# Kernel optimization log

Hardware: AMD Instinct MI355X
Metric: run time of the kernel (lower is better)

The kernel has to match this reference:

```python
import jax, jax.numpy as jnp
import numpy as np

IN_DIM, OUT_DIM = 96, 32
D = IN_DIM + OUT_DIM  # 128, feature dim of x
H, KQ = 8, 64         # head_num, KQ_dim
GAMMA = 1e-4


def setup_inputs() -> dict:
    key = jax.random.key(0)
    kx, kk, kq, kv = jax.random.split(key, 4)
    B, N = 32, 2048
    std_kq = (GAMMA / D) ** 0.5
    return {
        "x": jax.random.normal(kx, (B, N, D), dtype=jnp.float32),
        # nn.Linear weight shape [out_features, in_features]; stacked per head
        "Wk": jax.random.normal(kk, (H, KQ, D), dtype=jnp.float32) * std_kq,
        "Wq": jax.random.normal(kq, (H, KQ, D), dtype=jnp.float32) * std_kq,
        "Wv": jax.random.normal(kv, (H, D, D), dtype=jnp.float32) * GAMMA,
    }


def reference(x, Wk, Wq, Wv):
    # Per-head projections (nn.Linear: y = x @ W^T), stacked over heads h
    K = jnp.einsum("bnd,hkd->bhnk", x, Wk)  # [B,H,N,KQ]
    Q = jnp.einsum("bnd,hkd->bhnk", x, Wq)  # [B,H,N,KQ]
    V = jnp.einsum("bnd,hed->bhne", x, Wv)  # [B,H,N,D]
    # No softmax -> (Q K^T) V == Q (K^T V); use the O(n d^2) associative form
    KtV = jnp.einsum("bhnk,bhne->bhke", K, V)  # [B,H,KQ,D]
    # sum over heads folded into the contraction
    out = jnp.einsum("bhnk,bhke->bne", Q, KtV)  # [B,N,D]
    return out
```

## Files before the change

### kernel.cpp

```cpp
#include <hip/hip_runtime.h>

#define BB 32
#define NN 2048
#define DD 128
#define HH 8
#define KK 64

typedef __attribute__((ext_vector_type(8))) short bf16x8;
typedef __attribute__((ext_vector_type(4))) float f32x4;
#define MFMA_BF16 __builtin_amdgcn_mfma_f32_16x16x32_bf16


__device__ __forceinline__ float bf2f(unsigned short h){ return __uint_as_float(((unsigned)h) << 16); }
__device__ __forceinline__ unsigned short f2bf(float f){
  unsigned u = __float_as_uint(f);
  u += 0x7fffu + ((u >> 16) & 1u);
  return (unsigned short)(u >> 16);
}
__device__ __forceinline__ unsigned pack2(float a, float b){
  return (unsigned)f2bf(a) | ((unsigned)f2bf(b) << 16);
}

__device__ __forceinline__ bf16x8 ldfrag_sw(const unsigned short* base, int row16, int kc, int lane){
  int d = row16 + (lane & 15);
  int q = lane >> 4;
  int ch = ((kc << 2) + q) ^ (d & 7);
  return *(const bf16x8*)(base + d*128 + ch*8);
}

__global__ __launch_bounds__(512, 4) void kgkp(const float* __restrict__ x,
                                               const float* __restrict__ Wq,
                                               const float* __restrict__ Wk,
                                               unsigned short* __restrict__ Gp_bf,
                                               unsigned short* __restrict__ Pbf){
  __shared__ __align__(16) unsigned short sm[32768];
  const int t = threadIdx.x;
  const int bid = blockIdx.x;
  const int w = t >> 6, lane = t & 63, quad = lane >> 4;
  if (bid < 256){
    unsigned short* xh = sm;
    unsigned short* xl = sm + 16384;
    const int b = bid & 31, chunk = bid >> 5;
    const int wr = (w >> 1)*32, wc = (w & 1)*64;
    f32x4 acc[2][4] = {};
    for (int sub = 0; sub < 2; ++sub){
      if (sub) __syncthreads();
      const float* xb = x + ((size_t)b*NN + (size_t)(chunk*256 + sub*128))*DD;
      for (int it = 0; it < 2; ++it){
        int gidx = it*512 + t;
        int n4g = (gidx & 7) | (((gidx >> 6) & 3) << 3);
        int dcq = ((gidx >> 3) & 7) | (((gidx >> 8) & 3) << 3);
        float4 v[4];
        #pragma unroll
        for (int j = 0; j < 4; ++j)
          v[j] = *(const float4*)(xb + (size_t)(n4g*4 + j)*DD + dcq*4);
        #pragma unroll
        for (int i = 0; i < 4; ++i){
          int d = dcq*4 + i;
          float f0 = (&v[0].x)[i], f1 = (&v[1].x)[i], f2 = (&v[2].x)[i], f3 = (&v[3].x)[i];
          unsigned short h0 = f2bf(f0), h1 = f2bf(f1), h2 = f2bf(f2), h3 = f2bf(f3);
          unsigned short l0 = f2bf(f0 - bf2f(h0)), l1 = f2bf(f1 - bf2f(h1));
          unsigned short l2 = f2bf(f2 - bf2f(h2)), l3 = f2bf(f3 - bf2f(h3));
          int off = d*128 + ((((n4g >> 1) ^ (d & 7)) << 3) + (n4g & 1)*4);
          *(ushort4*)(xh + off) = make_ushort4(h0, h1, h2, h3);
          *(ushort4*)(xl + off) = make_ushort4(l0, l1, l2, l3);
        }
      }
      __syncthreads();
      for (int kc = 0; kc < 4; ++kc){
        bf16x8 ah[2], al[2], bh[4], bl[4];
        #pragma unroll
        for (int r = 0; r < 2; ++r){
          ah[r] = ldfrag_sw(xh, wr + r*16, kc, lane);
          al[r] = ldfrag_sw(xl, wr + r*16, kc, lane);
        }
        #pragma unroll
        for (int c = 0; c < 4; ++c){
          bh[c] = ldfrag_sw(xh, wc + c*16, kc, lane);
          bl[c] = ldfrag_sw(xl, wc + c*16, kc, lane);
        }
        #pragma unroll
        for (int r = 0; r < 2; ++r)
          #pragma unroll
          for (int c = 0; c < 4; ++c){
            acc[r][c] = MFMA_BF16(ah[r], bh[c], acc[r][c], 0, 0, 0);
            acc[r][c] = MFMA_BF16(ah[r], bl[c], acc[r][c], 0, 0, 0);
            acc[r][c] = MFMA_BF16(al[r], bh[c], acc[r][c], 0, 0, 0);
          }
      }
    }
    __syncthreads();
    float* Sf = (float*)sm;
    #pragma unroll
    for (int r = 0; r < 2; ++r)
      #pragma unroll
      for (int c = 0; c < 4; ++c)
        #pragma unroll
        for (int reg = 0; reg < 4; ++reg)
          Sf[(wr + r*16 + quad*4 + reg)*128 + wc + c*16 + (lane & 15)] = acc[r][c][reg];
    __syncthreads();
    unsigned short* gp = Gp_bf + ((size_t)(chunk*32 + b) << 14);
    for (int i = t; i < 2048; i += 512){
      int r = i >> 4, c8 = (i & 15) * 8;
      const float* s = Sf + r*128 + c8;
      uint4 o;
      o.x = pack2(s[0], s[1]); o.y = pack2(s[2], s[3]);
      o.z = pack2(s[4], s[5]); o.w = pack2(s[6], s[7]);
      *(uint4*)(gp + r*128 + c8) = o;
    }
  } else {
    float* Aq = (float*)sm;
    float* Bk = Aq + 64*36;
    const int kpid = bid - 256;
    const int h = kpid >> 2, rt = kpid & 3;
    const int i0 = rt * 32;
    const int tr = t >> 6, tc = t & 63;
    const float* wq = Wq + h*KK*DD;
    const float* wk = Wk + h*KK*DD;
    for (int i = t; i < 512; i += 512){
      int k = i >> 3, c4 = (i & 7) << 2;
      *(float4*)(&Aq[k*36 + c4]) = *(const float4*)(wq + k*DD + i0 + c4);
    }
    for (int i = t; i < 2048; i += 512){
      int k = i >> 5, c4 = (i & 31) << 2;
      *(float4*)(&Bk[k*132 + c4]) = *(const float4*)(wk + k*DD + c4);
    }
    __syncthreads();
    float acc[4][2] = {};
    for (int k = 0; k < 64; k += 2){
      float a0[4], a1[4], b0[2], b1[2];
      *(float4*)a0 = *(float4*)(&Aq[k*36 + tr*4]);
      *(float4*)a1 = *(float4*)(&Aq[(k+1)*36 + tr*4]);
      b0[0] = Bk[k*132 + tc*2];     b0[1] = Bk[k*132 + tc*2 + 1];
      b1[0] = Bk[(k+1)*132 + tc*2]; b1[1] = Bk[(k+1)*132 + tc*2 + 1];
      #pragma unroll
      for (int i = 0; i < 4; ++i)
        #pragma unroll
        for (int j = 0; j < 2; ++j){
          acc[i][j] += a0[i]*b0[j];
          acc[i][j] += a1[i]*b1[j];
        }
    }
    unsigned short* Ph = Pbf + h*DD*DD;
    #pragma unroll
    for (int i = 0; i < 4; ++i)
      *(ushort2*)(&Ph[(i0 + tr*4 + i)*DD + tc*2]) =
          make_ushort2(f2bf(acc[i][0]), f2bf(acc[i][1]));
  }
}

__global__ __launch_bounds__(512, 2) void km2(const unsigned short* __restrict__ Gp_bf,
                                              const float* __restrict__ Wv,
                                              const unsigned short* __restrict__ Pbf,
                                              unsigned short* __restrict__ Mp_bf){
  __shared__ __align__(16) unsigned short sm[32768];
  unsigned short* As = sm;
  unsigned short* Bs = sm + 16384;
  const int bid = blockIdx.x;
  const int b = bid & 31, h = bid >> 5;
  const int t = threadIdx.x;
  const int w = t >> 6, lane = t & 63, quad = lane >> 4;
  for (int i = t; i < 2048; i += 512){
    int r = i >> 4, c8 = (i & 15) * 8;
    float s[8] = {};
    #pragma unroll
    for (int p = 0; p < 8; ++p){
      uint4 u = *(const uint4*)(Gp_bf + (((size_t)(p*32 + b)) << 14) + r*128 + c8);
      const unsigned short* pu = (const unsigned short*)&u;
      #pragma unroll
      for (int j = 0; j < 8; ++j) s[j] += bf2f(pu[j]);
    }
    uint4 o;
    o.x = pack2(s[0], s[1]); o.y = pack2(s[2], s[3]);
    o.z = pack2(s[4], s[5]); o.w = pack2(s[6], s[7]);
    *(uint4*)(As + r*128 + ((((c8 >> 3) ^ (r & 7))) << 3)) = o;
  }
  const float* Wvh = Wv + (size_t)h*DD*DD;
  for (int i = t; i < 4096; i += 512){
    int e = i >> 5, dc = (i & 31) * 4;
    float4 v = *(const float4*)(Wvh + (size_t)e*DD + dc);
    int off = e*128 + ((((dc >> 3) ^ (e & 7)) << 3) + (dc & 4));
    *(ushort4*)(Bs + off) = make_ushort4(f2bf(v.x), f2bf(v.y), f2bf(v.z), f2bf(v.w));
  }
  __syncthreads();
  f32x4 acc1[8] = {};
  for (int kc = 0; kc < 4; ++kc){
    bf16x8 a = ldfrag_sw(As, w*16, kc, lane);
    bf16x8 bb[8];
    #pragma unroll
    for (int c = 0; c < 8; ++c) bb[c] = ldfrag_sw(Bs, c*16, kc, lane);
    #pragma unroll
    for (int c = 0; c < 8; ++c) acc1[c] = MFMA_BF16(a, bb[c], acc1[c], 0, 0, 0);
  }
  __syncthreads();
  #pragma unroll
  for (int c = 0; c < 8; ++c){
    int e = c*16 + (lane & 15);
    int d0 = w*16 + quad*4;
    int off = e*128 + ((((d0 >> 3) ^ (e & 7)) << 3) + (d0 & 7));
    *(ushort4*)(Bs + off) = make_ushort4(f2bf(acc1[c][0]), f2bf(acc1[c][1]),
                                         f2bf(acc1[c][2]), f2bf(acc1[c][3]));
  }
  const unsigned short* Ph = Pbf + (size_t)h*DD*DD;
  for (int i = t; i < 2048; i += 512){
    int r = i >> 4, ch = i & 15;
    *(uint4*)(As + r*128 + ((ch ^ (r & 7)) << 3)) = *(const uint4*)(Ph + r*128 + ch*8);
  }
  __syncthreads();
  f32x4 acc2[8] = {};
  for (int kc = 0; kc < 4; ++kc){
    bf16x8 a = ldfrag_sw(As, w*16, kc, lane);
    bf16x8 bb[8];
    #pragma unroll
    for (int c = 0; c < 8; ++c) bb[c] = ldfrag_sw(Bs, c*16, kc, lane);
    #pragma unroll
    for (int c = 0; c < 8; ++c) acc2[c] = MFMA_BF16(a, bb[c], acc2[c], 0, 0, 0);
  }
  __syncthreads();
  float* Sf = (float*)sm;
  #pragma unroll
  for (int c = 0; c < 8; ++c)
    #pragma unroll
    for (int reg = 0; reg < 4; ++reg)
      Sf[(w*16 + quad*4 + reg)*128 + c*16 + (lane & 15)] = acc2[c][reg];
  __syncthreads();
  unsigned short* Mb = Mp_bf + (((size_t)(b*8 + h)) << 14);
  for (int i = t; i < 2048; i += 512){
    int r = i >> 4, c8 = (i & 15) * 8;
    const float* s = Sf + r*128 + c8;
    uint4 o;
    o.x = pack2(s[0], s[1]); o.y = pack2(s[2], s[3]);
    o.z = pack2(s[4], s[5]); o.w = pack2(s[6], s[7]);
    *(uint4*)(Mb + r*128 + c8) = o;
  }
}

__global__ __launch_bounds__(256) void kmr(const unsigned short* __restrict__ Mp_bf,
                                           unsigned short* __restrict__ Mtbf){
  __shared__ float Sf[16][132];
  const int bid = blockIdx.x;
  const int b = bid >> 3, es = bid & 7;
  const int t = threadIdx.x;
  {
    int d = t >> 1, half = t & 1;
    float s[8] = {};
    #pragma unroll
    for (int h = 0; h < 8; ++h){
      uint4 u = *(const uint4*)(Mp_bf + (((size_t)(b*8 + h)) << 14) + d*128 + es*16 + half*8);
      const unsigned short* pu = (const unsigned short*)&u;
      #pragma unroll
      for (int j = 0; j < 8; ++j) s[j] += bf2f(pu[j]);
    }
    #pragma unroll
    for (int j = 0; j < 8; ++j) Sf[half*8 + j][d] = s[j];
  }
  __syncthreads();
  unsigned short* Mb = Mtbf + ((size_t)b << 14);
  for (int j = t; j < 2048; j += 256){
    int e = j >> 7, d = j & 127;
    Mb[(es*16 + e)*128 + d] = f2bf(Sf[e][d]);
  }
}

__global__ __launch_bounds__(512, 4) void ko2(const float* __restrict__ x,
                                              const unsigned short* __restrict__ Mtbf,
                                              float* __restrict__ out){
  __shared__ __align__(16) unsigned short sm[32768];
  unsigned short* xs = sm;
  unsigned short* Ms = sm + 16384;
  const int bid = blockIdx.x;
  const int b = bid & 31, nt = bid >> 5;
  const int t = threadIdx.x;
  const int w = t >> 6, lane = t & 63, quad = lane >> 4;
  const float* xb = x + ((size_t)b*NN + (size_t)nt*128)*DD;
  const unsigned short* Mtb = Mtbf + ((size_t)b << 14);
  for (int i = t; i < 4096; i += 512){
    int n = i >> 5, dcq = i & 31;
    float4 v = *(const float4*)(xb + (size_t)n*DD + dcq*4);
    int off = n*128 + ((((dcq >> 1) ^ (n & 7)) << 3) + (dcq & 1)*4);
    *(ushort4*)(xs + off) = make_ushort4(f2bf(v.x), f2bf(v.y), f2bf(v.z), f2bf(v.w));
  }
  for (int i = t; i < 2048; i += 512){
    int e = i >> 4, ng = i & 15;
    *(uint4*)(Ms + e*128 + ((ng ^ (e & 7)) << 3)) = *(const uint4*)(Mtb + e*128 + ng*8);
  }
  __syncthreads();
  const int wr = (w >> 1)*32, wc = (w & 1)*64;
  f32x4 acc[2][4] = {};
  for (int kc = 0; kc < 4; ++kc){
    bf16x8 a[2], bb[4];
    #pragma unroll
    for (int r = 0; r < 2; ++r) a[r] = ldfrag_sw(xs, wr + r*16, kc, lane);
    #pragma unroll
    for (int c = 0; c < 4; ++c) bb[c] = ldfrag_sw(Ms, wc + c*16, kc, lane);
    #pragma unroll
    for (int r = 0; r < 2; ++r)
      #pragma unroll
      for (int c = 0; c < 4; ++c)
        acc[r][c] = MFMA_BF16(a[r], bb[c], acc[r][c], 0, 0, 0);
  }
  __syncthreads();
  float* Sf = (float*)sm;
  #pragma unroll
  for (int r = 0; r < 2; ++r)
    #pragma unroll
    for (int c = 0; c < 4; ++c)
      #pragma unroll
      for (int reg = 0; reg < 4; ++reg)
        Sf[(wr + r*16 + quad*4 + reg)*128 + wc + c*16 + (lane & 15)] = acc[r][c][reg];
  __syncthreads();
  float* ob = out + ((size_t)b*NN + (size_t)nt*128)*DD;
  for (int i = t; i < 4096; i += 512){
    int n = i >> 5, c4 = (i & 31) * 4;
    *(float4*)(ob + (size_t)n*DD + c4) = *(const float4*)(Sf + n*128 + c4);
  }
}

extern "C" void kernel_launch(void* const* d_in, const int* in_sizes, int n_in,
                              void* d_out, int out_size, void* d_ws, size_t ws_size,
                              hipStream_t stream){
  const float* x  = (const float*)d_in[0];
  const float* Wk = (const float*)d_in[1];
  const float* Wq = (const float*)d_in[2];
  const float* Wv = (const float*)d_in[3];
  float* out = (float*)d_out;
  unsigned short* wsu = (unsigned short*)d_ws;
  unsigned short* Gp_bf = wsu;
  unsigned short* Mp_bf = wsu + 4194304;
  unsigned short* Pbf   = wsu + 8388608;
  unsigned short* Mtbf  = wsu + 8519680;

  kgkp<<<288, 512, 0, stream>>>(x, Wq, Wk, Gp_bf, Pbf);
  km2 <<<256, 512, 0, stream>>>(Gp_bf, Wv, Pbf, Mp_bf);
  kmr <<<256, 256, 0, stream>>>(Mp_bf, Mtbf);
  ko2 <<<512, 512, 0, stream>>>(x, Mtbf, out);
}
```

Measured before the change: 123.8 us.

## Cache bf16 x from first pass and pre-reduce G/Wv in a new kernel

The first kernel now also writes the bf16 high part of x to workspace in the swizzled tile layout. The output kernel then loads these 16-bit tiles directly instead of re-reading and converting the fp32 x, which roughly halves its input traffic. A new kernel kgr reduces the 8 partial G tiles once per batch and converts Wv to swizzled bf16 once per head, instead of repeating this in each of the 256 km2 blocks. P and Mt are also stored pre-swizzled so later loads become plain vector copies. The cost is an extra kernel launch and an extra 16 MB write of x_bf.

Measured after the change: 126.2 us. No clear change (+1.9%).

```diff
diff --git a/kernel.cpp b/kernel.cpp
--- a/kernel.cpp
+++ b/kernel.cpp
@@ -32,7 +32,8 @@
                                                const float* __restrict__ Wq,
                                                const float* __restrict__ Wk,
                                                unsigned short* __restrict__ Gp_bf,
-                                               unsigned short* __restrict__ Pbf){
+                                               unsigned short* __restrict__ Pbf,
+                                               unsigned short* __restrict__ x_bf){
   __shared__ __align__(16) unsigned short sm[32768];
   const int t = threadIdx.x;
   const int bid = blockIdx.x;
@@ -46,6 +47,7 @@
     for (int sub = 0; sub < 2; ++sub){
       if (sub) __syncthreads();
       const float* xb = x + ((size_t)b*NN + (size_t)(chunk*256 + sub*128))*DD;
+      unsigned short* xbo = x_bf + (((size_t)(b*16 + chunk*2 + sub)) << 14);
       for (int it = 0; it < 2; ++it){
         int gidx = it*512 + t;
         int n4g = (gidx & 7) | (((gidx >> 6) & 3) << 3);
@@ -54,16 +56,28 @@
         #pragma unroll
         for (int j = 0; j < 4; ++j)
           v[j] = *(const float4*)(xb + (size_t)(n4g*4 + j)*DD + dcq*4);
+        unsigned short hh[4][4], ll[4][4];
+        #pragma unroll
+        for (int j = 0; j < 4; ++j)
+          #pragma unroll
+          for (int i = 0; i < 4; ++i){
+            float f = (&v[j].x)[i];
+            unsigned short h = f2bf(f);
+            hh[j][i] = h;
+            ll[j][i] = f2bf(f - bf2f(h));
+          }
         #pragma unroll
         for (int i = 0; i < 4; ++i){
           int d = dcq*4 + i;
-          float f0 = (&v[0].x)[i], f1 = (&v[1].x)[i], f2 = (&v[2].x)[i], f3 = (&v[3].x)[i];
-          unsigned short h0 = f2bf(f0), h1 = f2bf(f1), h2 = f2bf(f2), h3 = f2bf(f3);
-          unsigned short l0 = f2bf(f0 - bf2f(h0)), l1 = f2bf(f1 - bf2f(h1));
-          unsigned short l2 = f2bf(f2 - bf2f(h2)), l3 = f2bf(f3 - bf2f(h3));
           int off = d*128 + ((((n4g >> 1) ^ (d & 7)) << 3) + (n4g & 1)*4);
-          *(ushort4*)(xh + off) = make_ushort4(h0, h1, h2, h3);
-          *(ushort4*)(xl + off) = make_ushort4(l0, l1, l2, l3);
+          *(ushort4*)(xh + off) = make_ushort4(hh[0][i], hh[1][i], hh[2][i], hh[3][i]);
+          *(ushort4*)(xl + off) = make_ushort4(ll[0][i], ll[1][i], ll[2][i], ll[3][i]);
+        }
+        #pragma unroll
+        for (int j = 0; j < 4; ++j){
+          int n = n4g*4 + j;
+          int off = n*128 + ((((dcq >> 1) ^ (n & 7)) << 3) + (dcq & 1)*4);
+          *(ushort4*)(xbo + off) = make_ushort4(hh[j][0], hh[j][1], hh[j][2], hh[j][3]);
         }
       }
       __syncthreads();
@@ -143,14 +157,49 @@
     }
     unsigned short* Ph = Pbf + h*DD*DD;
     #pragma unroll
-    for (int i = 0; i < 4; ++i)
-      *(ushort2*)(&Ph[(i0 + tr*4 + i)*DD + tc*2]) =
-          make_ushort2(f2bf(acc[i][0]), f2bf(acc[i][1]));
-  }
-}
-
-__global__ __launch_bounds__(512, 2) void km2(const unsigned short* __restrict__ Gp_bf,
-                                              const float* __restrict__ Wv,
+    for (int i = 0; i < 4; ++i){
+      int r = i0 + tr*4 + i, c = tc*2;
+      int off = r*128 + ((((c >> 3) ^ (r & 7)) << 3) + (c & 7));
+      *(ushort2*)(&Ph[off]) = make_ushort2(f2bf(acc[i][0]), f2bf(acc[i][1]));
+    }
+  }
+}
+
+__global__ __launch_bounds__(256) void kgr(const unsigned short* __restrict__ Gp_bf,
+                                           const float* __restrict__ Wv,
+                                           unsigned short* __restrict__ G_bf,
+                                           unsigned short* __restrict__ Wv_bf){
+  const int bid = blockIdx.x, t = threadIdx.x;
+  if (bid < 256){
+    const int b = bid >> 3, strip = bid & 7;
+    const int r = strip*16 + (t >> 4), ch = t & 15;
+    float s[8] = {};
+    #pragma unroll
+    for (int p = 0; p < 8; ++p){
+      uint4 u = *(const uint4*)(Gp_bf + (((size_t)(p*32 + b)) << 14) + r*128 + ch*8);
+      const unsigned short* pu = (const unsigned short*)&u;
+      #pragma unroll
+      for (int j = 0; j < 8; ++j) s[j] += bf2f(pu[j]);
+    }
+    uint4 o;
+    o.x = pack2(s[0], s[1]); o.y = pack2(s[2], s[3]);
+    o.z = pack2(s[4], s[5]); o.w = pack2(s[6], s[7]);
+    *(uint4*)(G_bf + ((size_t)b << 14) + r*128 + ((ch ^ (r & 7)) << 3)) = o;
+  } else {
+    const int h = bid - 256;
+    const float* Wvh = Wv + (size_t)h*DD*DD;
+    unsigned short* outp = Wv_bf + (size_t)h*DD*DD;
+    for (int i = t; i < 4096; i += 256){
+      int e = i >> 5, dc = (i & 31) * 4;
+      float4 v = *(const float4*)(Wvh + (size_t)e*DD + dc);
+      int off = e*128 + ((((dc >> 3) ^ (e & 7)) << 3) + (dc & 4));
+      *(ushort4*)(outp + off) = make_ushort4(f2bf(v.x), f2bf(v.y), f2bf(v.z), f2bf(v.w));
+    }
+  }
+}
+
+__global__ __launch_bounds__(512, 2) void km2(const unsigned short* __restrict__ G_bf,
+                                              const unsigned short* __restrict__ Wv_bf,
                                               const unsigned short* __restrict__ Pbf,
                                               unsigned short* __restrict__ Mp_bf){
   __shared__ __align__(16) unsigned short sm[32768];
@@ -160,27 +209,11 @@
   const int b = bid & 31, h = bid >> 5;
   const int t = threadIdx.x;
   const int w = t >> 6, lane = t & 63, quad = lane >> 4;
+  const unsigned short* Gb = G_bf + ((size_t)b << 14);
+  const unsigned short* Wvh = Wv_bf + ((size_t)h << 14);
   for (int i = t; i < 2048; i += 512){
-    int r = i >> 4, c8 = (i & 15) * 8;
-    float s[8] = {};
-    #pragma unroll
-    for (int p = 0; p < 8; ++p){
-      uint4 u = *(const uint4*)(Gp_bf + (((size_t)(p*32 + b)) << 14) + r*128 + c8);
-      const unsigned short* pu = (const unsigned short*)&u;
-      #pragma unroll
-      for (int j = 0; j < 8; ++j) s[j] += bf2f(pu[j]);
-    }
-    uint4 o;
-    o.x = pack2(s[0], s[1]); o.y = pack2(s[2], s[3]);
-    o.z = pack2(s[4], s[5]); o.w = pack2(s[6], s[7]);
-    *(uint4*)(As + r*128 + ((((c8 >> 3) ^ (r & 7))) << 3)) = o;
-  }
-  const float* Wvh = Wv + (size_t)h*DD*DD;
-  for (int i = t; i < 4096; i += 512){
-    int e = i >> 5, dc = (i & 31) * 4;
-    float4 v = *(const float4*)(Wvh + (size_t)e*DD + dc);
-    int off = e*128 + ((((dc >> 3) ^ (e & 7)) << 3) + (dc & 4));
-    *(ushort4*)(Bs + off) = make_ushort4(f2bf(v.x), f2bf(v.y), f2bf(v.z), f2bf(v.w));
+    *(uint4*)(As + i*8) = *(const uint4*)(Gb + i*8);
+    *(uint4*)(Bs + i*8) = *(const uint4*)(Wvh + i*8);
   }
   __syncthreads();
   f32x4 acc1[8] = {};
@@ -202,10 +235,8 @@
                                          f2bf(acc1[c][2]), f2bf(acc1[c][3]));
   }
   const unsigned short* Ph = Pbf + (size_t)h*DD*DD;
-  for (int i = t; i < 2048; i += 512){
-    int r = i >> 4, ch = i & 15;
-    *(uint4*)(As + r*128 + ((ch ^ (r & 7)) << 3)) = *(const uint4*)(Ph + r*128 + ch*8);
-  }
+  for (int i = t; i < 2048; i += 512)
+    *(uint4*)(As + i*8) = *(const uint4*)(Ph + i*8);
   __syncthreads();
   f32x4 acc2[8] = {};
   for (int kc = 0; kc < 4; ++kc){
@@ -236,7 +267,7 @@
 }
 
 __global__ __launch_bounds__(256) void kmr(const unsigned short* __restrict__ Mp_bf,
-                                           unsigned short* __restrict__ Mtbf){
+                                           unsigned short* __restrict__ Mt_sw){
   __shared__ float Sf[16][132];
   const int bid = blockIdx.x;
   const int b = bid >> 3, es = bid & 7;
@@ -255,15 +286,20 @@
     for (int j = 0; j < 8; ++j) Sf[half*8 + j][d] = s[j];
   }
   __syncthreads();
-  unsigned short* Mb = Mtbf + ((size_t)b << 14);
-  for (int j = t; j < 2048; j += 256){
-    int e = j >> 7, d = j & 127;
-    Mb[(es*16 + e)*128 + d] = f2bf(Sf[e][d]);
-  }
-}
-
-__global__ __launch_bounds__(512, 4) void ko2(const float* __restrict__ x,
-                                              const unsigned short* __restrict__ Mtbf,
+  unsigned short* Mb = Mt_sw + ((size_t)b << 14);
+  {
+    int el = t >> 4, ng = t & 15;
+    int e = es*16 + el;
+    const float* s = &Sf[el][ng*8];
+    uint4 o;
+    o.x = pack2(s[0], s[1]); o.y = pack2(s[2], s[3]);
+    o.z = pack2(s[4], s[5]); o.w = pack2(s[6], s[7]);
+    *(uint4*)(Mb + e*128 + ((ng ^ (e & 7)) << 3)) = o;
+  }
+}
+
+__global__ __launch_bounds__(512, 4) void ko2(const unsigned short* __restrict__ x_bf,
+                                              const unsigned short* __restrict__ Mt_sw,
                                               float* __restrict__ out){
   __shared__ __align__(16) unsigned short sm[32768];
   unsigned short* xs = sm;
@@ -272,17 +308,11 @@
   const int b = bid & 31, nt = bid >> 5;
   const int t = threadIdx.x;
   const int w = t >> 6, lane = t & 63, quad = lane >> 4;
-  const float* xb = x + ((size_t)b*NN + (size_t)nt*128)*DD;
-  const unsigned short* Mtb = Mtbf + ((size_t)b << 14);
-  for (int i = t; i < 4096; i += 512){
-    int n = i >> 5, dcq = i & 31;
-    float4 v = *(const float4*)(xb + (size_t)n*DD + dcq*4);
-    int off = n*128 + ((((dcq >> 1) ^ (n & 7)) << 3) + (dcq & 1)*4);
-    *(ushort4*)(xs + off) = make_ushort4(f2bf(v.x), f2bf(v.y), f2bf(v.z), f2bf(v.w));
-  }
+  const unsigned short* xbf = x_bf + (((size_t)(b*16 + nt)) << 14);
+  const unsigned short* Mtb = Mt_sw + ((size_t)b << 14);
   for (int i = t; i < 2048; i += 512){
-    int e = i >> 4, ng = i & 15;
-    *(uint4*)(Ms + e*128 + ((ng ^ (e & 7)) << 3)) = *(const uint4*)(Mtb + e*128 + ng*8);
+    *(uint4*)(xs + i*8) = *(const uint4*)(xbf + i*8);
+    *(uint4*)(Ms + i*8) = *(const uint4*)(Mtb + i*8);
   }
   __syncthreads();
   const int wr = (w >> 1)*32, wc = (w & 1)*64;
@@ -326,12 +356,16 @@
   float* out = (float*)d_out;
   unsigned short* wsu = (unsigned short*)d_ws;
   unsigned short* Gp_bf = wsu;
-  unsigned short* Mp_bf = wsu + 4194304;
-  unsigned short* Pbf   = wsu + 8388608;
-  unsigned short* Mtbf  = wsu + 8519680;
-
-  kgkp<<<288, 512, 0, stream>>>(x, Wq, Wk, Gp_bf, Pbf);
-  km2 <<<256, 512, 0, stream>>>(Gp_bf, Wv, Pbf, Mp_bf);
-  kmr <<<256, 256, 0, stream>>>(Mp_bf, Mtbf);
-  ko2 <<<512, 512, 0, stream>>>(x, Mtbf, out);
-}
+  unsigned short* G_bf  = wsu + 4194304;
+  unsigned short* Pbf   = wsu + 4718592;
+  unsigned short* Wv_bf = wsu + 4849664;
+  unsigned short* Mp_bf = wsu + 4980736;
+  unsigned short* Mt_sw = wsu + 9175040;
+  unsigned short* x_bf  = wsu + 9699328;
+
+  kgkp<<<288, 512, 0, stream>>>(x, Wq, Wk, Gp_bf, Pbf, x_bf);
+  kgr <<<264, 256, 0, stream>>>(Gp_bf, Wv, G_bf, Wv_bf);
+  km2 <<<256, 512, 0, stream>>>(G_bf, Wv_bf, Pbf, Mp_bf);
+  kmr <<<256, 256, 0, stream>>>(Mp_bf, Mt_sw);
+  ko2 <<<512, 512, 0, stream>>>(x_bf, Mt_sw, out);
+}
```

## Prefetch second x tile during MFMA, swizzle fp32 staging, preload P early

Applied to the files above, without the earlier changes.

In kgkp, the global loads for the second 128-row x sub-tile are issued before the first MFMA pass so their latency overlaps compute. This costs more registers, and the launch-bounds occupancy hint drops from 4 to 2 blocks per CU to allow for it. The fp32 staging buffer used for the accumulator write-out gets an XOR column swizzle in all three kernels to cut LDS bank conflicts. In km2, the P matrix is loaded into registers at kernel start instead of after the first GEMM, hiding that global load behind the Gp reduction and first MFMA phase.

New measurement: 129.5 us. 1.05x slower.

```diff
diff --git a/kernel.cpp b/kernel.cpp
--- a/kernel.cpp
+++ b/kernel.cpp
@@ -28,7 +28,9 @@
   return *(const bf16x8*)(base + d*128 + ch*8);
 }
 
-__global__ __launch_bounds__(512, 4) void kgkp(const float* __restrict__ x,
+__device__ __forceinline__ int sfswz(int row, int col){ return col ^ (((row >> 2) & 1) << 4); }
+
+__global__ __launch_bounds__(512, 2) void kgkp(const float* __restrict__ x,
                                                const float* __restrict__ Wq,
                                                const float* __restrict__ Wk,
                                                unsigned short* __restrict__ Gp_bf,
@@ -43,30 +45,40 @@
     const int b = bid & 31, chunk = bid >> 5;
     const int wr = (w >> 1)*32, wc = (w & 1)*64;
     f32x4 acc[2][4] = {};
-    for (int sub = 0; sub < 2; ++sub){
-      if (sub) __syncthreads();
-      const float* xb = x + ((size_t)b*NN + (size_t)(chunk*256 + sub*128))*DD;
+    int n4g[2], dcq[2];
+    #pragma unroll
+    for (int it = 0; it < 2; ++it){
+      int gidx = it*512 + t;
+      n4g[it] = (gidx & 7) | (((gidx >> 6) & 3) << 3);
+      dcq[it] = ((gidx >> 3) & 7) | (((gidx >> 8) & 3) << 3);
+    }
+    const float* xb0 = x + ((size_t)b*NN + (size_t)(chunk*256))*DD;
+    const float* xb1 = xb0 + (size_t)128*DD;
+    float4 v[2][4];
+
+    auto cvt_store = [&](){
+      #pragma unroll
       for (int it = 0; it < 2; ++it){
-        int gidx = it*512 + t;
-        int n4g = (gidx & 7) | (((gidx >> 6) & 3) << 3);
-        int dcq = ((gidx >> 3) & 7) | (((gidx >> 8) & 3) << 3);
-        float4 v[4];
+        unsigned short hh[4][4], ll[4][4];
         #pragma unroll
         for (int j = 0; j < 4; ++j)
-          v[j] = *(const float4*)(xb + (size_t)(n4g*4 + j)*DD + dcq*4);
+          #pragma unroll
+          for (int i = 0; i < 4; ++i){
+            float f = (&v[it][j].x)[i];
+            unsigned short h = f2bf(f);
+            hh[j][i] = h;
+            ll[j][i] = f2bf(f - bf2f(h));
+          }
         #pragma unroll
         for (int i = 0; i < 4; ++i){
-          int d = dcq*4 + i;
-          float f0 = (&v[0].x)[i], f1 = (&v[1].x)[i], f2 = (&v[2].x)[i], f3 = (&v[3].x)[i];
-          unsigned short h0 = f2bf(f0), h1 = f2bf(f1), h2 = f2bf(f2), h3 = f2bf(f3);
-          unsigned short l0 = f2bf(f0 - bf2f(h0)), l1 = f2bf(f1 - bf2f(h1));
-          unsigned short l2 = f2bf(f2 - bf2f(h2)), l3 = f2bf(f3 - bf2f(h3));
-          int off = d*128 + ((((n4g >> 1) ^ (d & 7)) << 3) + (n4g & 1)*4);
-          *(ushort4*)(xh + off) = make_ushort4(h0, h1, h2, h3);
-          *(ushort4*)(xl + off) = make_ushort4(l0, l1, l2, l3);
+          int d = dcq[it]*4 + i;
+          int off = d*128 + ((((n4g[it] >> 1) ^ (d & 7)) << 3) + (n4g[it] & 1)*4);
+          *(ushort4*)(xh + off) = make_ushort4(hh[0][i], hh[1][i], hh[2][i], hh[3][i]);
+          *(ushort4*)(xl + off) = make_ushort4(ll[0][i], ll[1][i], ll[2][i], ll[3][i]);
         }
       }
-      __syncthreads();
+    };
+    auto mfma_pass = [&](){
       for (int kc = 0; kc < 4; ++kc){
         bf16x8 ah[2], al[2], bh[4], bl[4];
         #pragma unroll
@@ -88,21 +100,42 @@
             acc[r][c] = MFMA_BF16(al[r], bh[c], acc[r][c], 0, 0, 0);
           }
       }
-    }
-    __syncthreads();
+    };
+
+    #pragma unroll
+    for (int it = 0; it < 2; ++it)
+      #pragma unroll
+      for (int j = 0; j < 4; ++j)
+        v[it][j] = *(const float4*)(xb0 + (size_t)(n4g[it]*4 + j)*DD + dcq[it]*4);
+    cvt_store();
+    #pragma unroll
+    for (int it = 0; it < 2; ++it)
+      #pragma unroll
+      for (int j = 0; j < 4; ++j)
+        v[it][j] = *(const float4*)(xb1 + (size_t)(n4g[it]*4 + j)*DD + dcq[it]*4);
+    __syncthreads();
+    mfma_pass();
+    __syncthreads();
+    cvt_store();
+    __syncthreads();
+    mfma_pass();
+    __syncthreads();
+
     float* Sf = (float*)sm;
     #pragma unroll
     for (int r = 0; r < 2; ++r)
       #pragma unroll
       for (int c = 0; c < 4; ++c)
         #pragma unroll
-        for (int reg = 0; reg < 4; ++reg)
-          Sf[(wr + r*16 + quad*4 + reg)*128 + wc + c*16 + (lane & 15)] = acc[r][c][reg];
+        for (int reg = 0; reg < 4; ++reg){
+          int row = wr + r*16 + quad*4 + reg;
+          Sf[row*128 + sfswz(row, wc + c*16 + (lane & 15))] = acc[r][c][reg];
+        }
     __syncthreads();
     unsigned short* gp = Gp_bf + ((size_t)(chunk*32 + b) << 14);
     for (int i = t; i < 2048; i += 512){
       int r = i >> 4, c8 = (i & 15) * 8;
-      const float* s = Sf + r*128 + c8;
+      const float* s = Sf + r*128 + sfswz(r, c8);
       uint4 o;
       o.x = pack2(s[0], s[1]); o.y = pack2(s[2], s[3]);
       o.z = pack2(s[4], s[5]); o.w = pack2(s[6], s[7]);
@@ -160,6 +193,11 @@
   const int b = bid & 31, h = bid >> 5;
   const int t = threadIdx.x;
   const int w = t >> 6, lane = t & 63, quad = lane >> 4;
+  const unsigned short* Ph = Pbf + (size_t)h*DD*DD;
+  uint4 preg[4];
+  #pragma unroll
+  for (int ri = 0; ri < 4; ++ri)
+    preg[ri] = *(const uint4*)(Ph + (size_t)(ri*512 + t)*8);
   for (int i = t; i < 2048; i += 512){
     int r = i >> 4, c8 = (i & 15) * 8;
     float s[8] = {};
@@ -201,10 +239,11 @@
     *(ushort4*)(Bs + off) = make_ushort4(f2bf(acc1[c][0]), f2bf(acc1[c][1]),
                                          f2bf(acc1[c][2]), f2bf(acc1[c][3]));
   }
-  const unsigned short* Ph = Pbf + (size_t)h*DD*DD;
-  for (int i = t; i < 2048; i += 512){
+  #pragma unroll
+  for (int ri = 0; ri < 4; ++ri){
+    int i = ri*512 + t;
     int r = i >> 4, ch = i & 15;
-    *(uint4*)(As + r*128 + ((ch ^ (r & 7)) << 3)) = *(const uint4*)(Ph + r*128 + ch*8);
+    *(uint4*)(As + r*128 + ((ch ^ (r & 7)) << 3)) = preg[ri];
   }
   __syncthreads();
   f32x4 acc2[8] = {};
@@ -221,13 +260,15 @@
   #pragma unroll
   for (int c = 0; c < 8; ++c)
     #pragma unroll
-    for (int reg = 0; reg < 4; ++reg)
-      Sf[(w*16 + quad*4 + reg)*128 + c*16 + (lane & 15)] = acc2[c][reg];
+    for (int reg = 0; reg < 4; ++reg){
+      int row = w*16 + quad*4 + reg;
+      Sf[row*128 + sfswz(row, c*16 + (lane & 15))] = acc2[c][reg];
+    }
   __syncthreads();
   unsigned short* Mb = Mp_bf + (((size_t)(b*8 + h)) << 14);
   for (int i = t; i < 2048; i += 512){
     int r = i >> 4, c8 = (i & 15) * 8;
-    const float* s = Sf + r*128 + c8;
+    const float* s = Sf + r*128 + sfswz(r, c8);
     uint4 o;
     o.x = pack2(s[0], s[1]); o.y = pack2(s[2], s[3]);
     o.z = pack2(s[4], s[5]); o.w = pack2(s[6], s[7]);
@@ -306,13 +347,15 @@
     #pragma unroll
     for (int c = 0; c < 4; ++c)
       #pragma unroll
-      for (int reg = 0; reg < 4; ++reg)
-        Sf[(wr + r*16 + quad*4 + reg)*128 + wc + c*16 + (lane & 15)] = acc[r][c][reg];
+      for (int reg = 0; reg < 4; ++reg){
+        int row = wr + r*16 + quad*4 + reg;
+        Sf[row*128 + sfswz(row, wc + c*16 + (lane & 15))] = acc[r][c][reg];
+      }
   __syncthreads();
   float* ob = out + ((size_t)b*NN + (size_t)nt*128)*DD;
   for (int i = t; i < 4096; i += 512){
     int n = i >> 5, c4 = (i & 31) * 4;
-    *(float4*)(ob + (size_t)n*DD + c4) = *(const float4*)(Sf + n*128 + c4);
+    *(float4*)(ob + (size_t)n*DD + c4) = *(const float4*)(Sf + n*128 + sfswz(n, c4));
   }
 }
 
```

## Fuse head-sum reduction into output GEMM and store transposed M from km2

Applied to the files above, without the earlier changes.

Removes the separate kmr kernel that summed per-head M matrices and transposed them. km2 now writes each head's M already transposed, going through an XOR-swizzled shared buffer with float4 reads. ko2 sums the 8 heads while it loads its M tile. This saves one launch and one global round trip, but every ko2 block (16 per batch) now re-reads 8 head slices, which adds redundant L2 traffic.

After: 120.8 us (median of 2 runs). 2.4% less time.

```diff
diff --git a/kernel.cpp b/kernel.cpp
--- a/kernel.cpp
+++ b/kernel.cpp
@@ -152,7 +152,7 @@
 __global__ __launch_bounds__(512, 2) void km2(const unsigned short* __restrict__ Gp_bf,
                                               const float* __restrict__ Wv,
                                               const unsigned short* __restrict__ Pbf,
-                                              unsigned short* __restrict__ Mp_bf){
+                                              unsigned short* __restrict__ Mp_t){
   __shared__ __align__(16) unsigned short sm[32768];
   unsigned short* As = sm;
   unsigned short* Bs = sm + 16384;
@@ -219,51 +219,31 @@
   __syncthreads();
   float* Sf = (float*)sm;
   #pragma unroll
-  for (int c = 0; c < 8; ++c)
-    #pragma unroll
-    for (int reg = 0; reg < 4; ++reg)
-      Sf[(w*16 + quad*4 + reg)*128 + c*16 + (lane & 15)] = acc2[c][reg];
-  __syncthreads();
-  unsigned short* Mb = Mp_bf + (((size_t)(b*8 + h)) << 14);
+  for (int c = 0; c < 8; ++c){
+    int e = c*16 + (lane & 15);
+    int xr = (e & 7) << 2;
+    #pragma unroll
+    for (int reg = 0; reg < 4; ++reg){
+      int d = w*16 + quad*4 + reg;
+      Sf[e*128 + (d ^ xr)] = acc2[c][reg];
+    }
+  }
+  __syncthreads();
+  unsigned short* Mb = Mp_t + (((size_t)(b*8 + h)) << 14);
   for (int i = t; i < 2048; i += 512){
-    int r = i >> 4, c8 = (i & 15) * 8;
-    const float* s = Sf + r*128 + c8;
+    int e = i >> 4, c8 = (i & 15) * 8;
+    int xr = (e & 7) << 2;
+    float4 lo = *(const float4*)(Sf + e*128 + (c8 ^ xr));
+    float4 hi = *(const float4*)(Sf + e*128 + ((c8 + 4) ^ xr));
     uint4 o;
-    o.x = pack2(s[0], s[1]); o.y = pack2(s[2], s[3]);
-    o.z = pack2(s[4], s[5]); o.w = pack2(s[6], s[7]);
-    *(uint4*)(Mb + r*128 + c8) = o;
-  }
-}
-
-__global__ __launch_bounds__(256) void kmr(const unsigned short* __restrict__ Mp_bf,
-                                           unsigned short* __restrict__ Mtbf){
-  __shared__ float Sf[16][132];
-  const int bid = blockIdx.x;
-  const int b = bid >> 3, es = bid & 7;
-  const int t = threadIdx.x;
-  {
-    int d = t >> 1, half = t & 1;
-    float s[8] = {};
-    #pragma unroll
-    for (int h = 0; h < 8; ++h){
-      uint4 u = *(const uint4*)(Mp_bf + (((size_t)(b*8 + h)) << 14) + d*128 + es*16 + half*8);
-      const unsigned short* pu = (const unsigned short*)&u;
-      #pragma unroll
-      for (int j = 0; j < 8; ++j) s[j] += bf2f(pu[j]);
-    }
-    #pragma unroll
-    for (int j = 0; j < 8; ++j) Sf[half*8 + j][d] = s[j];
-  }
-  __syncthreads();
-  unsigned short* Mb = Mtbf + ((size_t)b << 14);
-  for (int j = t; j < 2048; j += 256){
-    int e = j >> 7, d = j & 127;
-    Mb[(es*16 + e)*128 + d] = f2bf(Sf[e][d]);
+    o.x = pack2(lo.x, lo.y); o.y = pack2(lo.z, lo.w);
+    o.z = pack2(hi.x, hi.y); o.w = pack2(hi.z, hi.w);
+    *(uint4*)(Mb + e*128 + c8) = o;
   }
 }
 
 __global__ __launch_bounds__(512, 4) void ko2(const float* __restrict__ x,
-                                              const unsigned short* __restrict__ Mtbf,
+                                              const unsigned short* __restrict__ Mp_t,
                                               float* __restrict__ out){
   __shared__ __align__(16) unsigned short sm[32768];
   unsigned short* xs = sm;
@@ -273,16 +253,27 @@
   const int t = threadIdx.x;
   const int w = t >> 6, lane = t & 63, quad = lane >> 4;
   const float* xb = x + ((size_t)b*NN + (size_t)nt*128)*DD;
-  const unsigned short* Mtb = Mtbf + ((size_t)b << 14);
   for (int i = t; i < 4096; i += 512){
     int n = i >> 5, dcq = i & 31;
     float4 v = *(const float4*)(xb + (size_t)n*DD + dcq*4);
     int off = n*128 + ((((dcq >> 1) ^ (n & 7)) << 3) + (dcq & 1)*4);
     *(ushort4*)(xs + off) = make_ushort4(f2bf(v.x), f2bf(v.y), f2bf(v.z), f2bf(v.w));
   }
+  const unsigned short* Mpb = Mp_t + (((size_t)b * 8) << 14);
   for (int i = t; i < 2048; i += 512){
-    int e = i >> 4, ng = i & 15;
-    *(uint4*)(Ms + e*128 + ((ng ^ (e & 7)) << 3)) = *(const uint4*)(Mtb + e*128 + ng*8);
+    int e = i >> 4, dch = i & 15;
+    float s[8] = {};
+    #pragma unroll
+    for (int hh = 0; hh < 8; ++hh){
+      uint4 u = *(const uint4*)(Mpb + ((size_t)hh << 14) + e*128 + dch*8);
+      const unsigned short* pu = (const unsigned short*)&u;
+      #pragma unroll
+      for (int j = 0; j < 8; ++j) s[j] += bf2f(pu[j]);
+    }
+    uint4 o;
+    o.x = pack2(s[0], s[1]); o.y = pack2(s[2], s[3]);
+    o.z = pack2(s[4], s[5]); o.w = pack2(s[6], s[7]);
+    *(uint4*)(Ms + e*128 + ((dch ^ (e & 7)) << 3)) = o;
   }
   __syncthreads();
   const int wr = (w >> 1)*32, wc = (w & 1)*64;
@@ -326,12 +317,10 @@
   float* out = (float*)d_out;
   unsigned short* wsu = (unsigned short*)d_ws;
   unsigned short* Gp_bf = wsu;
-  unsigned short* Mp_bf = wsu + 4194304;
+  unsigned short* Mp_t  = wsu + 4194304;
   unsigned short* Pbf   = wsu + 8388608;
-  unsigned short* Mtbf  = wsu + 8519680;
 
   kgkp<<<288, 512, 0, stream>>>(x, Wq, Wk, Gp_bf, Pbf);
-  km2 <<<256, 512, 0, stream>>>(Gp_bf, Wv, Pbf, Mp_bf);
-  kmr <<<256, 256, 0, stream>>>(Mp_bf, Mtbf);
-  ko2 <<<512, 512, 0, stream>>>(x, Mtbf, out);
-}
+  km2 <<<256, 512, 0, stream>>>(Gp_bf, Wv, Pbf, Mp_t);
+  ko2 <<<512, 512, 0, stream>>>(x, Mp_t, out);
+}
```
